# Performance work log

Measured on AMD Instinct MI355X. Metric: run time of the kernel, lower is better.

## Reference

```python
import jax, jax.numpy as jnp
import numpy as np

HIDDEN = 1024
NUM_HEADS = 16
HEAD_DIM = HIDDEN // NUM_HEADS  # 64
GRID_SIZE = 5
SPLINE_ORDER = 3
GRID_LO, GRID_HI = -1.0, 1.0


def b_splines(x2d, grid, k=SPLINE_ORDER):
    # x2d: (N, in), grid: (in, GRID_SIZE + 2k + 1) -> (N, in, GRID_SIZE + k)
    xg = x2d[:, :, None]
    g = grid[None, :, :]
    bases = ((xg >= g[:, :, :-1]) & (xg < g[:, :, 1:])).astype(x2d.dtype)
    for j in range(1, k + 1):
        left = (xg - g[:, :, : -(j + 1)]) / (g[:, :, j:-1] - g[:, :, : -(j + 1)]) * bases[:, :, :-1]
        right = (g[:, :, j + 1 :] - xg) / (g[:, :, j + 1 :] - g[:, :, 1:-j]) * bases[:, :, 1:]
        bases = left + right
    return bases


def setup_inputs() -> dict:
    key = jax.random.key(0)
    ks = jax.random.split(key, 6)
    B, S = 1, 2048
    in_f, out_f = HIDDEN, 3 * HIDDEN
    x = jax.random.normal(ks[0], (B, S, HIDDEN), dtype=jnp.float32)
    base_weight = jax.random.normal(ks[1], (out_f, in_f), dtype=jnp.float32) * (1.0 / np.sqrt(in_f))
    n_coef = GRID_SIZE + SPLINE_ORDER  # 8
    spline_weight = jax.random.normal(ks[2], (out_f, in_f, n_coef), dtype=jnp.float32) * 0.1
    spline_scaler = jnp.ones((out_f, in_f), dtype=jnp.float32)
    out_w = jax.random.normal(ks[3], (HIDDEN, HIDDEN), dtype=jnp.float32) * (1.0 / np.sqrt(HIDDEN))
    out_b = jnp.zeros((HIDDEN,), dtype=jnp.float32)
    # extended B-spline grid, same for every input feature
    h = (GRID_HI - GRID_LO) / GRID_SIZE
    grid_row = jnp.arange(-SPLINE_ORDER, GRID_SIZE + SPLINE_ORDER + 1, dtype=jnp.float32) * h + GRID_LO
    grid = jnp.tile(grid_row[None, :], (in_f, 1))  # (in, GRID_SIZE + 2k + 1)
    # RoPE rotation matrix (cos/sin of pos * theta), theta base 10000
    half = HEAD_DIM // 2
    inv_freq = 1.0 / (10000.0 ** (jnp.arange(0, half, dtype=jnp.float32) / half))
    angles = jnp.arange(S, dtype=jnp.float32)[:, None] * inv_freq[None, :]  # (S, half)
    rot_cos = jnp.cos(angles)
    rot_sin = jnp.sin(angles)
    return {"x": x, "base_weight": base_weight, "spline_weight": spline_weight,
            "spline_scaler": spline_scaler, "out_w": out_w, "out_b": out_b,
            "grid": grid, "rot_cos": rot_cos, "rot_sin": rot_sin}


def apply_rope(t, rot_cos, rot_sin):
    # t: (B, H, S, D); pairs (t[..., 2i], t[..., 2i+1]) viewed as complex, mult by cis
    tr = t[..., 0::2]
    ti = t[..., 1::2]
    c = rot_cos[None, None, :, :]
    s = rot_sin[None, None, :, :]
    nr = tr * c - ti * s
    ni = tr * s + ti * c
    return jnp.stack([nr, ni], axis=-1).reshape(t.shape)


def reference(x, base_weight, spline_weight, spline_scaler, out_w, out_b, grid, rot_cos, rot_sin):
    B, S, H = x.shape
    N = B * S
    x2 = x.reshape(N, H)
    # KANLinear: base branch + spline branch
    base = jax.nn.silu(x2) @ base_weight.T  # (N, 3H)
    bs = b_splines(x2, grid)  # (N, in, G+k)
    sw = (spline_weight * spline_scaler[:, :, None]).reshape(spline_weight.shape[0], -1)
    spline = bs.reshape(N, -1) @ sw.T
    qkv = (base + spline).reshape(B, S, NUM_HEADS, 3 * HEAD_DIM).transpose(0, 2, 1, 3)
    q, k, v = jnp.split(qkv, 3, axis=-1)  # each (B, nh, S, hd)
    q = apply_rope(q, rot_cos, rot_sin)
    k = apply_rope(k, rot_cos, rot_sin)
    scores = jnp.einsum("bhqd,bhkd->bhqk", q, k) / np.sqrt(HEAD_DIM).astype(np.float32)
    attn = jax.nn.softmax(scores, axis=-1)
    ctx = jnp.einsum("bhqk,bhkd->bhqd", attn, v)
    ctx = ctx.transpose(0, 2, 1, 3).reshape(B, S, H)
    return ctx @ out_w.T + out_b
```

## Files before the change

### kernel.cpp

```cpp
#include <hip/hip_runtime.h>

#define DEVI __device__ __forceinline__

typedef float f32x4 __attribute__((ext_vector_type(4)));
typedef __bf16 bf16x8 __attribute__((ext_vector_type(8)));

constexpr int S   = 2048;
constexpr int HID = 1024;
constexpr int HD  = 64;
constexpr int O3  = 3072;
constexpr int KF  = 9216;

DEVI unsigned short f2bf(float f) {
  unsigned int u = __float_as_uint(f);
  u = (u + 0x7FFFu + ((u >> 16) & 1u)) >> 16;
  return (unsigned short)u;
}
DEVI float b2f(unsigned int u) { return __uint_as_float(u << 16); }
DEVI float fexp(float x) { return __builtin_amdgcn_exp2f(x * 1.44269504089f); }

DEVI void gload16(const void* g, void* l) {
  __builtin_amdgcn_global_load_lds((const __attribute__((address_space(1))) void*)g,
                                   (__attribute__((address_space(3))) void*)l, 16, 0, 0);
}

__global__ __launch_bounds__(256) void kconv_w(const float* __restrict__ bw,
    const float* __restrict__ sw, const float* __restrict__ sc,
    unsigned short* __restrict__ Wc) {
  unsigned int t = blockIdx.x * 256 + threadIdx.x;
  unsigned int o = t / 1152, jc = t % 1152;
  unsigned int j = jc * 8;
  float v[8];
  if (j < 1024) {
    const float4* p = (const float4*)(bw + (size_t)o * 1024 + j);
    float4 a = p[0], b = p[1];
    v[0]=a.x; v[1]=a.y; v[2]=a.z; v[3]=a.w; v[4]=b.x; v[5]=b.y; v[6]=b.z; v[7]=b.w;
  } else {
    unsigned int i = (j - 1024) >> 3;
    float s = sc[(size_t)o * 1024 + i];
    const float4* p = (const float4*)(sw + ((size_t)o * 1024 + i) * 8);
    float4 a = p[0], b = p[1];
    v[0]=a.x*s; v[1]=a.y*s; v[2]=a.z*s; v[3]=a.w*s; v[4]=b.x*s; v[5]=b.y*s; v[6]=b.z*s; v[7]=b.w*s;
  }
  union { unsigned short u[8]; uint4 q; } pk;
  #pragma unroll
  for (int c = 0; c < 8; ++c) pk.u[c] = f2bf(v[c]);
  *(uint4*)(Wc + (size_t)o * KF + j) = pk.q;
}

__global__ __launch_bounds__(256) void kconv_outw(const float* __restrict__ ow,
    unsigned short* __restrict__ Wo) {
  unsigned int t = blockIdx.x * 256 + threadIdx.x;
  unsigned int o = t >> 7, j = (t & 127) * 8;
  const float4* p = (const float4*)(ow + (size_t)o * 1024 + j);
  float4 a = p[0], b = p[1];
  float v[8] = {a.x, a.y, a.z, a.w, b.x, b.y, b.z, b.w};
  union { unsigned short u[8]; uint4 q; } pk;
  #pragma unroll
  for (int c = 0; c < 8; ++c) pk.u[c] = f2bf(v[c]);
  *(uint4*)(Wo + (size_t)o * 1024 + j) = pk.q;
}

__global__ __launch_bounds__(256) void kfeatures(const float* __restrict__ x,
    const float* __restrict__ grid, unsigned short* __restrict__ F) {
  unsigned int t = blockIdx.x * 256 + threadIdx.x;
  unsigned int n = t >> 10, i = t & 1023;
  float xv = x[t];
  float sil = xv / (1.f + expf(-xv));
  F[(size_t)n * KF + i] = f2bf(sil);
  float g[12];
  #pragma unroll
  for (int j = 0; j < 12; ++j) g[j] = grid[i * 12 + j];
  float b[11];
  #pragma unroll
  for (int j = 0; j < 11; ++j) b[j] = (xv >= g[j] && xv < g[j + 1]) ? 1.f : 0.f;
  #pragma unroll
  for (int ord = 1; ord <= 3; ++ord)
    #pragma unroll
    for (int j = 0; j + ord < 11; ++j)
      b[j] = (xv - g[j]) / (g[j + ord] - g[j]) * b[j]
           + (g[j + ord + 1] - xv) / (g[j + ord + 1] - g[j + 1]) * b[j + 1];
  union { unsigned short u[8]; uint4 q; } pk;
  #pragma unroll
  for (int c = 0; c < 8; ++c) pk.u[c] = f2bf(b[c]);
  *(uint4*)(F + (size_t)n * KF + 1024 + i * 8) = pk.q;
}

__global__ __launch_bounds__(256) void kgemm_bt(const unsigned short* __restrict__ A,
    const unsigned short* __restrict__ W, void* __restrict__ C,
    const float* __restrict__ bias, int N, int nkPer, int mode) {
  const int bm = blockIdx.x, bn = blockIdx.y;
  const int tid = threadIdx.x;
  const int w = tid >> 6, lane = tid & 63;
  const int l16 = lane & 15, g4 = lane >> 4;
  const int wr = w >> 1, wc = w & 1;
  __shared__ __align__(16) unsigned short As[128 * 32];
  __shared__ __align__(16) unsigned short Bs[128 * 32];
  f32x4 acc[4][4] = {};
  const int K = (mode == 1) ? KF : 1024;
  const int koff = blockIdx.z * nkPer;
  for (int kt = koff; kt < koff + nkPer; ++kt) {
    #pragma unroll
    for (int r = 0; r < 2; ++r) {
      int chunk = r * 256 + w * 64 + lane;
      int row = chunk >> 2, col = (chunk & 3) * 8;
      int ldsoff = (r * 256 + w * 64) * 16;
      gload16(A + (size_t)(bm * 128 + row) * K + kt * 32 + col, (char*)As + ldsoff);
      gload16(W + (size_t)(bn * 128 + row) * K + kt * 32 + col, (char*)Bs + ldsoff);
    }
    asm volatile("s_waitcnt vmcnt(0)" ::: "memory");
    __syncthreads();
    bf16x8 af[4], bf[4];
    #pragma unroll
    for (int f = 0; f < 4; ++f)
      af[f] = *(const bf16x8*)(As + (wr * 64 + f * 16 + l16) * 32 + g4 * 8);
    #pragma unroll
    for (int f = 0; f < 4; ++f)
      bf[f] = *(const bf16x8*)(Bs + (wc * 64 + f * 16 + l16) * 32 + g4 * 8);
    #pragma unroll
    for (int fr = 0; fr < 4; ++fr)
      #pragma unroll
      for (int fc = 0; fc < 4; ++fc)
        acc[fr][fc] = __builtin_amdgcn_mfma_f32_16x16x32_bf16(af[fr], bf[fc], acc[fr][fc], 0, 0, 0);
    __syncthreads();
  }
  if (mode == 0) {
    float* Cf = (float*)C;
    #pragma unroll
    for (int fr = 0; fr < 4; ++fr) {
      int rowb = bm * 128 + wr * 64 + fr * 16 + g4 * 4;
      #pragma unroll
      for (int fc = 0; fc < 4; ++fc) {
        int col = bn * 128 + wc * 64 + fc * 16 + l16;
        float bv = bias[col];
        #pragma unroll
        for (int rg = 0; rg < 4; ++rg)
          Cf[(size_t)(rowb + rg) * N + col] = acc[fr][fc][rg] + bv;
      }
    }
  } else {
    unsigned short* Cb = (unsigned short*)C + (size_t)blockIdx.z * 2048 * N;
    #pragma unroll
    for (int fr = 0; fr < 4; ++fr) {
      int rowb = bm * 128 + wr * 64 + fr * 16 + g4 * 4;
      #pragma unroll
      for (int fc = 0; fc < 4; ++fc) {
        int col = bn * 128 + wc * 64 + fc * 16 + l16;
        #pragma unroll
        for (int rg = 0; rg < 4; ++rg)
          Cb[(size_t)(rowb + rg) * N + col] = f2bf(acc[fr][fc][rg]);
      }
    }
  }
}

__global__ __launch_bounds__(256) void krope_qk(const unsigned short* __restrict__ qA,
    const unsigned short* __restrict__ qB, const float* __restrict__ rc,
    const float* __restrict__ rs, unsigned short* __restrict__ Qb,
    unsigned short* __restrict__ Kb) {
  unsigned int t = blockIdx.x * 256 + threadIdx.x;
  int d = t & 31;
  int h = (t >> 5) & 15;
  int n = t >> 9;
  size_t base = (size_t)n * O3 + h * 192;
  unsigned int a0 = *(const unsigned int*)(qA + base + 2 * d);
  unsigned int a1 = *(const unsigned int*)(qB + base + 2 * d);
  unsigned int e0 = *(const unsigned int*)(qA + base + 64 + 2 * d);
  unsigned int e1 = *(const unsigned int*)(qB + base + 64 + 2 * d);
  float qr = b2f(a0 & 0xffffu) + b2f(a1 & 0xffffu);
  float qi = b2f(a0 >> 16)     + b2f(a1 >> 16);
  float kr = b2f(e0 & 0xffffu) + b2f(e1 & 0xffffu);
  float ki = b2f(e0 >> 16)     + b2f(e1 >> 16);
  float c = rc[n * 32 + d], sn = rs[n * 32 + d];
  unsigned int qp = (unsigned int)f2bf((qr * c - qi * sn) * 0.125f)
                  | ((unsigned int)f2bf((qr * sn + qi * c) * 0.125f) << 16);
  unsigned int kp = (unsigned int)f2bf(kr * c - ki * sn)
                  | ((unsigned int)f2bf(kr * sn + ki * c) << 16);
  *(unsigned int*)(Qb + (size_t)h * S * HD + (size_t)n * HD + 2 * d) = qp;
  *(unsigned int*)(Kb + (size_t)h * S * HD + (size_t)n * HD + 2 * d) = kp;
}

__global__ __launch_bounds__(256) void kpack_vt(const unsigned short* __restrict__ qA,
    const unsigned short* __restrict__ qB, unsigned short* __restrict__ Vt) {
  const int nt = blockIdx.x;
  const int h  = blockIdx.y;
  const int tid = threadIdx.x;
  __shared__ __align__(16) unsigned short T[64][72];
  const int n0 = nt * 64;
  #pragma unroll
  for (int it = 0; it < 2; ++it) {
    int idx = it * 256 + tid;
    int r = idx >> 3;
    int c8 = (idx & 7) * 8;
    size_t base = (size_t)(n0 + r) * O3 + h * 192 + 128 + c8;
    uint4 u0 = *(const uint4*)(qA + base);
    uint4 u1 = *(const uint4*)(qB + base);
    const unsigned short* p0 = (const unsigned short*)&u0;
    const unsigned short* p1 = (const unsigned short*)&u1;
    #pragma unroll
    for (int j = 0; j < 8; ++j)
      T[c8 + j][r] = f2bf(b2f(p0[j]) + b2f(p1[j]));
  }
  __syncthreads();
  #pragma unroll
  for (int it = 0; it < 2; ++it) {
    int idx = it * 256 + tid;
    int dd = idx >> 3;
    int c8 = (idx & 7) * 8;
    *(uint4*)(Vt + (size_t)h * HD * S + (size_t)dd * S + n0 + c8) = *(const uint4*)&T[dd][c8];
  }
}

__global__ __launch_bounds__(256) void kattn(const unsigned short* __restrict__ Qb,
    const unsigned short* __restrict__ Kb, const unsigned short* __restrict__ Vt,
    unsigned short* __restrict__ ctx) {
  const int qb = blockIdx.x, h = blockIdx.y;
  const int tid = threadIdx.x, w = tid >> 6, lane = tid & 63;
  const int l16 = lane & 15, g4 = lane >> 4;
  __shared__ __align__(16) unsigned short Ks[64 * 64];
  __shared__ __align__(16) unsigned short Vs[64 * 64];
  __shared__ __align__(16) unsigned short Ps[4][16 * 64];
  const unsigned short* Qh = Qb + (size_t)h * S * HD;
  const unsigned short* Kh = Kb + (size_t)h * S * HD;
  const unsigned short* Vh = Vt + (size_t)h * HD * S;
  bf16x8 qf[2];
  #pragma unroll
  for (int ks = 0; ks < 2; ++ks)
    qf[ks] = *(const bf16x8*)(Qh + (size_t)(qb * 64 + w * 16 + l16) * HD + ks * 32 + g4 * 8);
  f32x4 o[4] = {};
  float lp[4] = {0.f, 0.f, 0.f, 0.f};

  for (int t = 0; t < S / 64; ++t) {
    int kv0 = t * 64;
    #pragma unroll
    for (int r = 0; r < 2; ++r) {
      int chunk = r * 256 + w * 64 + lane;
      int row = chunk >> 3;
      int c8 = ((chunk ^ row) & 7) * 8;
      int ldsoff = (r * 256 + w * 64) * 16;
      gload16(Kh + (size_t)(kv0 + row) * HD + c8, (char*)Ks + ldsoff);
      gload16(Vh + (size_t)row * S + kv0 + c8, (char*)Vs + ldsoff);
    }
    asm volatile("s_waitcnt vmcnt(0)" ::: "memory");
    __syncthreads();
    f32x4 s[4] = {};
    #pragma unroll
    for (int fc = 0; fc < 4; ++fc) {
      int rw = fc * 16 + l16;
      #pragma unroll
      for (int ks = 0; ks < 2; ++ks) {
        bf16x8 bk = *(const bf16x8*)(Ks + rw * 64 + (((ks * 4 + g4) ^ (l16 & 7)) * 8));
        s[fc] = __builtin_amdgcn_mfma_f32_16x16x32_bf16(qf[ks], bk, s[fc], 0, 0, 0);
      }
    }
    #pragma unroll
    for (int fc = 0; fc < 4; ++fc)
      #pragma unroll
      for (int rg = 0; rg < 4; ++rg) {
        float p = fexp(s[fc][rg]);
        lp[rg] += p;
        int row = g4 * 4 + rg;
        Ps[w][row * 64 + ((fc * 2 + (l16 >> 3)) ^ (row & 7)) * 8 + (l16 & 7)] = f2bf(p);
      }
    #pragma unroll
    for (int ks = 0; ks < 2; ++ks) {
      bf16x8 ap = *(const bf16x8*)(Ps[w] + l16 * 64 + (((ks * 4 + g4) ^ (l16 & 7)) * 8));
      #pragma unroll
      for (int fc = 0; fc < 4; ++fc) {
        int rw = fc * 16 + l16;
        bf16x8 bv = *(const bf16x8*)(Vs + rw * 64 + (((ks * 4 + g4) ^ (l16 & 7)) * 8));
        o[fc] = __builtin_amdgcn_mfma_f32_16x16x32_bf16(ap, bv, o[fc], 0, 0, 0);
      }
    }
    __syncthreads();
  }
  #pragma unroll
  for (int rg = 0; rg < 4; ++rg) {
    float l = lp[rg];
    l += __shfl_xor(l, 1, 64);
    l += __shfl_xor(l, 2, 64);
    l += __shfl_xor(l, 4, 64);
    l += __shfl_xor(l, 8, 64);
    float inv = 1.f / l;
    int row = qb * 64 + w * 16 + g4 * 4 + rg;
    #pragma unroll
    for (int fc = 0; fc < 4; ++fc)
      ctx[(size_t)row * HID + h * HD + fc * 16 + l16] = f2bf(o[fc][rg] * inv);
  }
}

extern "C" void kernel_launch(void* const* d_in, const int* in_sizes, int n_in,
                              void* d_out, int out_size, void* d_ws, size_t ws_size,
                              hipStream_t stream) {
  const float* x    = (const float*)d_in[0];
  const float* bw   = (const float*)d_in[1];
  const float* sw   = (const float*)d_in[2];
  const float* sc   = (const float*)d_in[3];
  const float* ow   = (const float*)d_in[4];
  const float* ob   = (const float*)d_in[5];
  const float* grid = (const float*)d_in[6];
  const float* rc   = (const float*)d_in[7];
  const float* rs   = (const float*)d_in[8];
  float* out = (float*)d_out;
  char* ws = (char*)d_ws;

  unsigned short* F    = (unsigned short*)(ws);
  unsigned short* Wc   = (unsigned short*)(ws + 37748736);
  unsigned short* Wo   = (unsigned short*)(ws + 94371840);
  unsigned short* qkv0 = (unsigned short*)(ws + 96468992);
  unsigned short* qkv1 = qkv0 + (size_t)2048 * O3;
  unsigned short* Qb   = (unsigned short*)(ws + 121634816);
  unsigned short* Kb   = (unsigned short*)(ws + 125829120);
  unsigned short* Vt   = (unsigned short*)(ws + 130023424);
  unsigned short* ctx  = (unsigned short*)(ws + 134217728);

  kconv_w   <<<dim3(13824), dim3(256), 0, stream>>>(bw, sw, sc, Wc);
  kconv_outw<<<dim3(512),   dim3(256), 0, stream>>>(ow, Wo);
  kfeatures <<<dim3(8192),  dim3(256), 0, stream>>>(x, grid, F);
  kgemm_bt  <<<dim3(16, 24, 2), dim3(256), 0, stream>>>(F, Wc, qkv0, (const float*)nullptr, 3072, 144, 1);
  krope_qk  <<<dim3(4096),  dim3(256), 0, stream>>>(qkv0, qkv1, rc, rs, Qb, Kb);
  kpack_vt  <<<dim3(32, 16), dim3(256), 0, stream>>>(qkv0, qkv1, Vt);
  kattn     <<<dim3(32, 16), dim3(256), 0, stream>>>(Qb, Kb, Vt, ctx);
  kgemm_bt  <<<dim3(16, 8, 1),  dim3(256), 0, stream>>>(ctx, Wo, out, ob, 1024, 32, 0);
}
```

Baseline: 459.9 us.

## Swizzle split-K GEMM blocks, make split count adaptive, double-buffer attention K/V

The big KAN GEMM gets an XCD-aware block-index swizzle, and its split-K factor rises from 2 to 4 when the workspace is large enough. The rope and V-pack kernels are generalised to sum any number of partials. Attention now double-buffers K/V tiles in LDS, prefetching the next tile while computing the current one, and raises wave priority around the MFMA sections. The aim is better GEMM occupancy and cache locality and hiding attention load latency, at the cost of more partial-buffer traffic and extra LDS.

```diff
diff --git a/kernel.cpp b/kernel.cpp
--- a/kernel.cpp
+++ b/kernel.cpp
@@ -89,7 +89,18 @@
 __global__ __launch_bounds__(256) void kgemm_bt(const unsigned short* __restrict__ A,
     const unsigned short* __restrict__ W, void* __restrict__ C,
     const float* __restrict__ bias, int N, int nkPer, int mode) {
-  const int bm = blockIdx.x, bn = blockIdx.y;
+  int bm, bn, kz;
+  if (mode == 1) {
+    int gxy = gridDim.x * gridDim.y;
+    int nwg = gxy * gridDim.z;
+    int lin = blockIdx.x + gridDim.x * (blockIdx.y + gridDim.y * blockIdx.z);
+    int per = nwg >> 3;
+    int swz = (lin & 7) * per + (lin >> 3);
+    kz = swz / gxy;
+    int r = swz - kz * gxy;
+    bm = r / gridDim.y;
+    bn = r - bm * gridDim.y;
+  } else { bm = blockIdx.x; bn = blockIdx.y; kz = 0; }
   const int tid = threadIdx.x;
   const int w = tid >> 6, lane = tid & 63;
   const int l16 = lane & 15, g4 = lane >> 4;
@@ -98,7 +109,7 @@
   __shared__ __align__(16) unsigned short Bs[128 * 32];
   f32x4 acc[4][4] = {};
   const int K = (mode == 1) ? KF : 1024;
-  const int koff = blockIdx.z * nkPer;
+  const int koff = kz * nkPer;
   for (int kt = koff; kt < koff + nkPer; ++kt) {
     #pragma unroll
     for (int r = 0; r < 2; ++r) {
@@ -139,7 +150,7 @@
       }
     }
   } else {
-    unsigned short* Cb = (unsigned short*)C + (size_t)blockIdx.z * 2048 * N;
+    unsigned short* Cb = (unsigned short*)C + (size_t)kz * 2048 * N;
     #pragma unroll
     for (int fr = 0; fr < 4; ++fr) {
       int rowb = bm * 128 + wr * 64 + fr * 16 + g4 * 4;
@@ -154,34 +165,32 @@
   }
 }
 
-__global__ __launch_bounds__(256) void krope_qk(const unsigned short* __restrict__ qA,
-    const unsigned short* __restrict__ qB, const float* __restrict__ rc,
-    const float* __restrict__ rs, unsigned short* __restrict__ Qb,
-    unsigned short* __restrict__ Kb) {
+__global__ __launch_bounds__(256) void krope_qk(const unsigned short* __restrict__ qp,
+    int splits, const float* __restrict__ rc, const float* __restrict__ rs,
+    unsigned short* __restrict__ Qb, unsigned short* __restrict__ Kb) {
   unsigned int t = blockIdx.x * 256 + threadIdx.x;
   int d = t & 31;
   int h = (t >> 5) & 15;
   int n = t >> 9;
-  size_t base = (size_t)n * O3 + h * 192;
-  unsigned int a0 = *(const unsigned int*)(qA + base + 2 * d);
-  unsigned int a1 = *(const unsigned int*)(qB + base + 2 * d);
-  unsigned int e0 = *(const unsigned int*)(qA + base + 64 + 2 * d);
-  unsigned int e1 = *(const unsigned int*)(qB + base + 64 + 2 * d);
-  float qr = b2f(a0 & 0xffffu) + b2f(a1 & 0xffffu);
-  float qi = b2f(a0 >> 16)     + b2f(a1 >> 16);
-  float kr = b2f(e0 & 0xffffu) + b2f(e1 & 0xffffu);
-  float ki = b2f(e0 >> 16)     + b2f(e1 >> 16);
+  float qr = 0.f, qi = 0.f, kr = 0.f, ki = 0.f;
+  for (int p = 0; p < splits; ++p) {
+    size_t base = (size_t)p * 2048 * O3 + (size_t)n * O3 + h * 192;
+    unsigned int a = *(const unsigned int*)(qp + base + 2 * d);
+    unsigned int e = *(const unsigned int*)(qp + base + 64 + 2 * d);
+    qr += b2f(a & 0xffffu); qi += b2f(a >> 16);
+    kr += b2f(e & 0xffffu); ki += b2f(e >> 16);
+  }
   float c = rc[n * 32 + d], sn = rs[n * 32 + d];
-  unsigned int qp = (unsigned int)f2bf((qr * c - qi * sn) * 0.125f)
-                  | ((unsigned int)f2bf((qr * sn + qi * c) * 0.125f) << 16);
-  unsigned int kp = (unsigned int)f2bf(kr * c - ki * sn)
-                  | ((unsigned int)f2bf(kr * sn + ki * c) << 16);
-  *(unsigned int*)(Qb + (size_t)h * S * HD + (size_t)n * HD + 2 * d) = qp;
-  *(unsigned int*)(Kb + (size_t)h * S * HD + (size_t)n * HD + 2 * d) = kp;
-}
-
-__global__ __launch_bounds__(256) void kpack_vt(const unsigned short* __restrict__ qA,
-    const unsigned short* __restrict__ qB, unsigned short* __restrict__ Vt) {
+  unsigned int qpk = (unsigned int)f2bf((qr * c - qi * sn) * 0.125f)
+                   | ((unsigned int)f2bf((qr * sn + qi * c) * 0.125f) << 16);
+  unsigned int kpk = (unsigned int)f2bf(kr * c - ki * sn)
+                   | ((unsigned int)f2bf(kr * sn + ki * c) << 16);
+  *(unsigned int*)(Qb + (size_t)h * S * HD + (size_t)n * HD + 2 * d) = qpk;
+  *(unsigned int*)(Kb + (size_t)h * S * HD + (size_t)n * HD + 2 * d) = kpk;
+}
+
+__global__ __launch_bounds__(256) void kpack_vt(const unsigned short* __restrict__ qp,
+    int splits, unsigned short* __restrict__ Vt) {
   const int nt = blockIdx.x;
   const int h  = blockIdx.y;
   const int tid = threadIdx.x;
@@ -192,14 +201,16 @@
     int idx = it * 256 + tid;
     int r = idx >> 3;
     int c8 = (idx & 7) * 8;
-    size_t base = (size_t)(n0 + r) * O3 + h * 192 + 128 + c8;
-    uint4 u0 = *(const uint4*)(qA + base);
-    uint4 u1 = *(const uint4*)(qB + base);
-    const unsigned short* p0 = (const unsigned short*)&u0;
-    const unsigned short* p1 = (const unsigned short*)&u1;
-    #pragma unroll
-    for (int j = 0; j < 8; ++j)
-      T[c8 + j][r] = f2bf(b2f(p0[j]) + b2f(p1[j]));
+    float acc[8] = {};
+    for (int p = 0; p < splits; ++p) {
+      size_t base = (size_t)p * 2048 * O3 + (size_t)(n0 + r) * O3 + h * 192 + 128 + c8;
+      uint4 u = *(const uint4*)(qp + base);
+      const unsigned short* pu = (const unsigned short*)&u;
+      #pragma unroll
+      for (int j = 0; j < 8; ++j) acc[j] += b2f(pu[j]);
+    }
+    #pragma unroll
+    for (int j = 0; j < 8; ++j) T[c8 + j][r] = f2bf(acc[j]);
   }
   __syncthreads();
   #pragma unroll
@@ -217,8 +228,8 @@
   const int qb = blockIdx.x, h = blockIdx.y;
   const int tid = threadIdx.x, w = tid >> 6, lane = tid & 63;
   const int l16 = lane & 15, g4 = lane >> 4;
-  __shared__ __align__(16) unsigned short Ks[64 * 64];
-  __shared__ __align__(16) unsigned short Vs[64 * 64];
+  __shared__ __align__(16) unsigned short Ks[2][64 * 64];
+  __shared__ __align__(16) unsigned short Vs[2][64 * 64];
   __shared__ __align__(16) unsigned short Ps[4][16 * 64];
   const unsigned short* Qh = Qb + (size_t)h * S * HD;
   const unsigned short* Kh = Kb + (size_t)h * S * HD;
@@ -230,7 +241,7 @@
   f32x4 o[4] = {};
   float lp[4] = {0.f, 0.f, 0.f, 0.f};
 
-  for (int t = 0; t < S / 64; ++t) {
+  auto STAGE = [&](int buf, int t) {
     int kv0 = t * 64;
     #pragma unroll
     for (int r = 0; r < 2; ++r) {
@@ -238,21 +249,35 @@
       int row = chunk >> 3;
       int c8 = ((chunk ^ row) & 7) * 8;
       int ldsoff = (r * 256 + w * 64) * 16;
-      gload16(Kh + (size_t)(kv0 + row) * HD + c8, (char*)Ks + ldsoff);
-      gload16(Vh + (size_t)row * S + kv0 + c8, (char*)Vs + ldsoff);
-    }
-    asm volatile("s_waitcnt vmcnt(0)" ::: "memory");
+      gload16(Kh + (size_t)(kv0 + row) * HD + c8, (char*)Ks[buf] + ldsoff);
+      gload16(Vh + (size_t)row * S + kv0 + c8, (char*)Vs[buf] + ldsoff);
+    }
+  };
+
+  STAGE(0, 0);
+  int cur = 0;
+  for (int t = 0; t < S / 64; ++t) {
+    if (t + 1 < S / 64) {
+      STAGE(cur ^ 1, t + 1);
+      asm volatile("s_waitcnt vmcnt(4)" ::: "memory");
+    } else {
+      asm volatile("s_waitcnt vmcnt(0)" ::: "memory");
+    }
     __syncthreads();
+    const unsigned short* Kc = Ks[cur];
+    const unsigned short* Vc = Vs[cur];
     f32x4 s[4] = {};
+    __builtin_amdgcn_s_setprio(1);
     #pragma unroll
     for (int fc = 0; fc < 4; ++fc) {
       int rw = fc * 16 + l16;
       #pragma unroll
       for (int ks = 0; ks < 2; ++ks) {
-        bf16x8 bk = *(const bf16x8*)(Ks + rw * 64 + (((ks * 4 + g4) ^ (l16 & 7)) * 8));
+        bf16x8 bk = *(const bf16x8*)(Kc + rw * 64 + (((ks * 4 + g4) ^ (l16 & 7)) * 8));
         s[fc] = __builtin_amdgcn_mfma_f32_16x16x32_bf16(qf[ks], bk, s[fc], 0, 0, 0);
       }
     }
+    __builtin_amdgcn_s_setprio(0);
     #pragma unroll
     for (int fc = 0; fc < 4; ++fc)
       #pragma unroll
@@ -262,17 +287,20 @@
         int row = g4 * 4 + rg;
         Ps[w][row * 64 + ((fc * 2 + (l16 >> 3)) ^ (row & 7)) * 8 + (l16 & 7)] = f2bf(p);
       }
+    __builtin_amdgcn_s_setprio(1);
     #pragma unroll
     for (int ks = 0; ks < 2; ++ks) {
       bf16x8 ap = *(const bf16x8*)(Ps[w] + l16 * 64 + (((ks * 4 + g4) ^ (l16 & 7)) * 8));
       #pragma unroll
       for (int fc = 0; fc < 4; ++fc) {
         int rw = fc * 16 + l16;
-        bf16x8 bv = *(const bf16x8*)(Vs + rw * 64 + (((ks * 4 + g4) ^ (l16 & 7)) * 8));
+        bf16x8 bv = *(const bf16x8*)(Vc + rw * 64 + (((ks * 4 + g4) ^ (l16 & 7)) * 8));
         o[fc] = __builtin_amdgcn_mfma_f32_16x16x32_bf16(ap, bv, o[fc], 0, 0, 0);
       }
     }
+    __builtin_amdgcn_s_setprio(0);
     __syncthreads();
+    cur ^= 1;
   }
   #pragma unroll
   for (int rg = 0; rg < 4; ++rg) {
@@ -304,22 +332,25 @@
   float* out = (float*)d_out;
   char* ws = (char*)d_ws;
 
+  const size_t PARTIAL = (size_t)2048 * O3 * 2;
+  int splits = (ws_size >= (size_t)96468992 + 4 * PARTIAL + 4 * 4194304) ? 4 : 2;
+
   unsigned short* F    = (unsigned short*)(ws);
   unsigned short* Wc   = (unsigned short*)(ws + 37748736);
   unsigned short* Wo   = (unsigned short*)(ws + 94371840);
-  unsigned short* qkv0 = (unsigned short*)(ws + 96468992);
-  unsigned short* qkv1 = qkv0 + (size_t)2048 * O3;
-  unsigned short* Qb   = (unsigned short*)(ws + 121634816);
-  unsigned short* Kb   = (unsigned short*)(ws + 125829120);
-  unsigned short* Vt   = (unsigned short*)(ws + 130023424);
-  unsigned short* ctx  = (unsigned short*)(ws + 134217728);
+  unsigned short* qkvp = (unsigned short*)(ws + 96468992);
+  char* tail = ws + 96468992 + (size_t)splits * PARTIAL;
+  unsigned short* Qb   = (unsigned short*)(tail);
+  unsigned short* Kb   = (unsigned short*)(tail + 4194304);
+  unsigned short* Vt   = (unsigned short*)(tail + 8388608);
+  unsigned short* ctx  = (unsigned short*)(tail + 12582912);
 
   kconv_w   <<<dim3(13824), dim3(256), 0, stream>>>(bw, sw, sc, Wc);
   kconv_outw<<<dim3(512),   dim3(256), 0, stream>>>(ow, Wo);
   kfeatures <<<dim3(8192),  dim3(256), 0, stream>>>(x, grid, F);
-  kgemm_bt  <<<dim3(16, 24, 2), dim3(256), 0, stream>>>(F, Wc, qkv0, (const float*)nullptr, 3072, 144, 1);
-  krope_qk  <<<dim3(4096),  dim3(256), 0, stream>>>(qkv0, qkv1, rc, rs, Qb, Kb);
-  kpack_vt  <<<dim3(32, 16), dim3(256), 0, stream>>>(qkv0, qkv1, Vt);
+  kgemm_bt  <<<dim3(16, 24, splits), dim3(256), 0, stream>>>(F, Wc, qkvp, (const float*)nullptr, 3072, 288 / splits, 1);
+  krope_qk  <<<dim3(4096),  dim3(256), 0, stream>>>(qkvp, splits, rc, rs, Qb, Kb);
+  kpack_vt  <<<dim3(32, 16), dim3(256), 0, stream>>>(qkvp, splits, Vt);
   kattn     <<<dim3(32, 16), dim3(256), 0, stream>>>(Qb, Kb, Vt, ctx);
   kgemm_bt  <<<dim3(16, 8, 1),  dim3(256), 0, stream>>>(ctx, Wo, out, ob, 1024, 32, 0);
 }
```

Result: no change. 461.2 us (+0.3%).
